# Performance work log

Hardware: AMD Instinct MI355X
Metric: run time of the kernel (lower is better)

## Reference

```python
import math
import jax, jax.numpy as jnp
import numpy as np

NTYPE, C, H, E = 3, 256, 8, 32  # n_embd=256, n_head=8, edge_dim=32
A1 = 16  # aux_x1 feature dim (aux_x2 dim = E - A1)


def setup_inputs() -> dict:
    key = jax.random.key(0)
    ks = jax.random.split(key, 16)
    B, T1, T2 = 8, 128, 256
    s = 0.02
    return {
        "x1": jax.random.normal(ks[0], (B, T1, C), jnp.float32),
        "x2": jax.random.normal(ks[1], (B, T2, C), jnp.float32),
        "aux_x1": jax.random.normal(ks[2], (B, T1, A1), jnp.float32),
        "aux_x2": jax.random.normal(ks[3], (B, T2, E - A1), jnp.float32),
        "masks": jax.random.randint(ks[4], (NTYPE, B, T1, T2), 0, 2, jnp.int32),
        # per-type linear params, stored (in, out) so y = x @ W + b
        "Wq": jax.random.normal(ks[5], (NTYPE, C, C), jnp.float32) * s,
        "bq": jnp.zeros((NTYPE, C), jnp.float32),
        "Wk": jax.random.normal(ks[6], (NTYPE, C + E, C), jnp.float32) * s,
        "bk": jnp.zeros((NTYPE, C), jnp.float32),
        "Wv": jax.random.normal(ks[7], (NTYPE, C + E, C), jnp.float32) * s,
        "bv": jnp.zeros((NTYPE, C), jnp.float32),
        "Wp": jax.random.normal(ks[8], (NTYPE, C, C), jnp.float32) * s,
        "bp": jnp.zeros((NTYPE, C), jnp.float32),
    }


def _aux_attn(x1, x2, aux_x1, aux_x2, mask, Wq, bq, Wk, bk, Wv, bv, Wp, bp):
    """One AuxCrossAttention type. mask: (B,T1,T2) int."""
    B, T1, _ = x1.shape
    T2 = x2.shape[1]
    hd = C // H
    scale = 1.0 / math.sqrt(hd)

    q = x1 @ Wq + bq  # (B,T1,C)
    # k/v over aug_x2 = [x2 | aux_x1 | aux_x2]; split the linear instead of
    # materializing the (B,T1,T2,C+E) concat (same math by linearity).
    Wk_x, Wk_a1, Wk_a2 = Wk[:C], Wk[C:C + A1], Wk[C + A1:]
    Wv_x, Wv_a1, Wv_a2 = Wv[:C], Wv[C:C + A1], Wv[C + A1:]
    k = (x2 @ Wk_x + aux_x2 @ Wk_a2 + bk)[:, None] + (aux_x1 @ Wk_a1)[:, :, None]  # (B,T1,T2,C)
    v = (x2 @ Wv_x + aux_x2 @ Wv_a2 + bv)[:, None] + (aux_x1 @ Wv_a1)[:, :, None]  # (B,T1,T2,C)

    qh = q.reshape(B, T1, H, hd)
    kh = k.reshape(B, T1, T2, H, hd)
    vh = v.reshape(B, T1, T2, H, hd)

    att = jnp.einsum("bthd,btshd->bhts", qh, kh) * scale  # (B,H,T1,T2)
    valid = (mask != 0)[:, None]  # (B,1,T1,T2)
    att = jnp.where(valid, att, -jnp.inf)
    all_masked = (mask == 0).all(-1)  # (B,T1)
    att = jnp.where(all_masked[:, None, :, None], 0.0, att)
    f = jnp.finfo(att.dtype)
    att = jnp.nan_to_num(att, nan=0.0, posinf=f.max, neginf=f.min)
    att = jax.nn.softmax(att, axis=-1)

    y = jnp.einsum("bhts,btshd->bthd", att, vh).reshape(B, T1, C)
    return y @ Wp + bp


def reference(x1, x2, aux_x1, aux_x2, masks, Wq, bq, Wk, bk, Wv, bv, Wp, bp):
    resid = jnp.zeros_like(x1)
    for i in range(NTYPE):
        resid = resid + _aux_attn(x1, x2, aux_x1, aux_x2, masks[i],
                                  Wq[i], bq[i], Wk[i], bk[i], Wv[i], bv[i], Wp[i], bp[i])
    return resid
```

## Files before the change

### kernel.cpp

```cpp
#include <hip/hip_runtime.h>
#include <hip/hip_bf16.h>

#define NC 256
#define HD 32

typedef __attribute__((ext_vector_type(8))) short short8;
typedef __attribute__((ext_vector_type(4))) short short4v;
typedef __attribute__((ext_vector_type(4))) float f32x4;

#define QSC (0.17677669529663687f * 1.4426950408889634f)

__device__ __forceinline__ unsigned short f2bf(float f) {
    union { float f; unsigned u; } v; v.f = f;
    unsigned r = v.u + 0x7fffu + ((v.u >> 16) & 1u);
    return (unsigned short)(r >> 16);
}
__device__ __forceinline__ short8 cvt8(float4 a, float4 b) {
    short8 s;
    s[0] = (short)f2bf(a.x); s[1] = (short)f2bf(a.y);
    s[2] = (short)f2bf(a.z); s[3] = (short)f2bf(a.w);
    s[4] = (short)f2bf(b.x); s[5] = (short)f2bf(b.y);
    s[6] = (short)f2bf(b.z); s[7] = (short)f2bf(b.w);
    return s;
}

__global__ __launch_bounds__(256) void prep(
    const float* __restrict__ x1, const float* __restrict__ x2,
    const float* __restrict__ ax1, const float* __restrict__ ax2,
    const int* __restrict__ masks,
    const float* __restrict__ Wq, const float* __restrict__ Wk,
    const float* __restrict__ Wv, const float* __restrict__ Wp,
    short* __restrict__ x1b, short* __restrict__ A2, short* __restrict__ ax1p,
    unsigned int* __restrict__ mb,
    short* __restrict__ WqT, short* __restrict__ WkT, short* __restrict__ WvT,
    short* __restrict__ WpT)
{
    const int bx = blockIdx.x, tid = threadIdx.x;
    const short8 zero8 = {0, 0, 0, 0, 0, 0, 0, 0};

    if (bx < 64) {
        const size_t base = ((size_t)bx * 256 + tid) * 16;
        const float* p = x1 + base;
        float4 a = *(const float4*)p,       b = *(const float4*)(p + 4);
        float4 c = *(const float4*)(p + 8), d = *(const float4*)(p + 12);
        *(short8*)&x1b[base]     = cvt8(a, b);
        *(short8*)&x1b[base + 8] = cvt8(c, d);
    } else if (bx < 352) {
        const int g = (bx - 64) * 256 + tid;
        const int row = g / 36, c8 = g - row * 36;
        short8 s;
        if (c8 < 32) {
            const float* p = x2 + (size_t)row * 256 + c8 * 8;
            s = cvt8(*(const float4*)p, *(const float4*)(p + 4));
        } else if (c8 < 34) {
            const float* p = ax2 + (size_t)row * 16 + (c8 - 32) * 8;
            s = cvt8(*(const float4*)p, *(const float4*)(p + 4));
        } else {
            s = zero8;
        }
        *(short8*)&A2[(size_t)row * 288 + c8 * 8] = s;
    } else if (bx < 356) {
        const int row = (bx - 352) * 256 + tid;
        const float* p = ax1 + (size_t)row * 16;
        float4 a = *(const float4*)p,       b = *(const float4*)(p + 4);
        float4 c = *(const float4*)(p + 8), d = *(const float4*)(p + 12);
        short* o = ax1p + (size_t)row * 32;
        *(short8*)o        = cvt8(a, b);
        *(short8*)(o + 8)  = cvt8(c, d);
        *(short8*)(o + 16) = zero8;
        *(short8*)(o + 24) = zero8;
    } else if (bx < 548) {
        const int r0 = (bx - 356) * 16;
        const int wave = tid >> 6, lane = tid & 63;
        for (int rr = 0; rr < 16; ++rr) {
            const int row = r0 + rr;
            const int mk = masks[(size_t)row * 256 + tid];
            unsigned long long bal = __ballot(mk != 0);
            if (lane == 0) {
                mb[row * 8 + wave * 2 + 0] = (unsigned int)bal;
                mb[row * 8 + wave * 2 + 1] = (unsigned int)(bal >> 32);
            }
        }
    } else if (bx < 644) {
        const int idx = bx - 548, i = idx >> 5, k8 = idx & 31;
        const int n = tid;
        const float* W = Wq + (size_t)i * 256 * 256;
        short8 s;
#pragma unroll
        for (int j = 0; j < 8; ++j) s[j] = (short)f2bf(W[(size_t)(k8 * 8 + j) * 256 + n]);
        *(short8*)&WqT[(size_t)i * 256 * 256 + (size_t)n * 256 + k8 * 8] = s;
    } else if (bx < 860) {
        const int idx0 = bx - 644;
        const int kv = idx0 / 108, idx = idx0 % 108;
        const int i = idx / 36, k8 = idx % 36;
        const int n = tid;
        const float* W = (kv ? Wv : Wk) + (size_t)i * 288 * 256;
        short* O = (kv ? WvT : WkT) + (size_t)i * 256 * 288;
        short8 s;
#pragma unroll
        for (int j = 0; j < 8; ++j) {
            const int kp = k8 * 8 + j;
            const int src = (kp < 256) ? kp : (kp < 272 ? kp + 16 : -1);
            s[j] = (src >= 0) ? (short)f2bf(W[(size_t)src * 256 + n]) : (short)0;
        }
        *(short8*)&O[(size_t)n * 288 + k8 * 8] = s;
    } else {
        const int idx = bx - 860, i = idx >> 5, k8 = idx & 31;
        const int n = tid;
        const float* W = Wp + (size_t)i * 256 * 256;
        short8 s;
#pragma unroll
        for (int j = 0; j < 8; ++j) s[j] = (short)f2bf(W[(size_t)(k8 * 8 + j) * 256 + n]);
        *(short8*)&WpT[(size_t)i * 256 * 256 + (size_t)n * 256 + k8 * 8] = s;
    }
}

__global__ __launch_bounds__(256) void qkv_attn(
    const short* __restrict__ x1b, const short* __restrict__ A2,
    const short* __restrict__ WqT, const short* __restrict__ WkT,
    const short* __restrict__ WvT, const float* __restrict__ Wv,
    const short* __restrict__ WpT,
    const float* __restrict__ bq, const float* __restrict__ bk,
    const float* __restrict__ bv, const unsigned int* __restrict__ mb,
    short* __restrict__ yb, short* __restrict__ WeffT)
{
    const int tid = threadIdx.x;
    const int wave = tid >> 6, lane = tid & 63;
    const int qd = lane >> 4, ml = lane & 15;
    const int bx = blockIdx.x;

    if (bx == 192) {
        f32x4 wacc[4];
#pragma unroll
        for (int nt = 0; nt < 4; ++nt) wacc[nt] = {0.f, 0.f, 0.f, 0.f};
        for (int i = 0; i < 3; ++i) {
            const float* Wvp = Wv + (size_t)i * 288 * 256;
            const short* Wpt = WpT + (size_t)i * 256 * 256;
            for (int step = 0; step < 8; ++step) {
                const float* ap = Wvp + (size_t)(256 + ml) * 256 + step * 32 + qd * 8;
                short8 af = cvt8(*(const float4*)ap, *(const float4*)(ap + 4));
#pragma unroll
                for (int nt = 0; nt < 4; ++nt) {
                    const int n = (wave * 4 + nt) * 16 + ml;
                    short8 bf = *(const short8*)&Wpt[(size_t)n * 256 + step * 32 + qd * 8];
                    wacc[nt] = __builtin_amdgcn_mfma_f32_16x16x32_bf16(af, bf, wacc[nt], 0, 0, 0);
                }
            }
        }
#pragma unroll
        for (int nt = 0; nt < 4; ++nt) {
            const int n = (wave * 4 + nt) * 16 + ml;
#pragma unroll
            for (int r = 0; r < 4; ++r) {
                WeffT[n * 32 + qd * 4 + r] = (short)f2bf(wacc[nt][r]);
                WeffT[n * 32 + 16 + qd * 4 + r] = 0;
            }
        }
        return;
    }

    const int i = bx >> 6, b = (bx >> 3) & 7, h = bx & 7;
    const size_t bb = (size_t)i * 8 + b;
    const int hc = h * 32;

    __shared__ short q_s[128][40];
    __shared__ short k_s[256][40];
    __shared__ short vT_s[32][264];
    __shared__ short P_s[4][4096];

    const short* Wq_i = WqT + (size_t)i * 256 * 256;
    const short* Wk_i = WkT + (size_t)i * 256 * 288;
    const short* Wv_i = WvT + (size_t)i * 256 * 288;

    {
        f32x4 acc[2][2];
#pragma unroll
        for (int mt = 0; mt < 2; ++mt)
#pragma unroll
            for (int nt = 0; nt < 2; ++nt) acc[mt][nt] = {0.f, 0.f, 0.f, 0.f};
        for (int step = 0; step < 8; ++step) {
            short8 af[2], bf[2];
#pragma unroll
            for (int mt = 0; mt < 2; ++mt)
                af[mt] = *(const short8*)&x1b[(size_t)(b * 128 + wave * 32 + mt * 16 + ml) * 256 + step * 32 + qd * 8];
#pragma unroll
            for (int nt = 0; nt < 2; ++nt)
                bf[nt] = *(const short8*)&Wq_i[(size_t)(hc + nt * 16 + ml) * 256 + step * 32 + qd * 8];
#pragma unroll
            for (int mt = 0; mt < 2; ++mt)
#pragma unroll
                for (int nt = 0; nt < 2; ++nt)
                    acc[mt][nt] = __builtin_amdgcn_mfma_f32_16x16x32_bf16(af[mt], bf[nt], acc[mt][nt], 0, 0, 0);
        }
#pragma unroll
        for (int nt = 0; nt < 2; ++nt) {
            const float bsv = bq[i * 256 + hc + nt * 16 + ml];
#pragma unroll
            for (int mt = 0; mt < 2; ++mt) {
                const int r0 = wave * 32 + mt * 16 + qd * 4;
#pragma unroll
                for (int r = 0; r < 4; ++r)
                    q_s[r0 + r][nt * 16 + ml] = (short)f2bf((acc[mt][nt][r] + bsv) * QSC);
            }
        }
    }

    {
        f32x4 acc[4][2];
#pragma unroll
        for (int mt = 0; mt < 4; ++mt)
#pragma unroll
            for (int nt = 0; nt < 2; ++nt) acc[mt][nt] = {0.f, 0.f, 0.f, 0.f};
        for (int step = 0; step < 9; ++step) {
            short8 af[4], bf[2];
#pragma unroll
            for (int mt = 0; mt < 4; ++mt)
                af[mt] = *(const short8*)&A2[(size_t)(b * 256 + wave * 64 + mt * 16 + ml) * 288 + step * 32 + qd * 8];
#pragma unroll
            for (int nt = 0; nt < 2; ++nt)
                bf[nt] = *(const short8*)&Wk_i[(size_t)(hc + nt * 16 + ml) * 288 + step * 32 + qd * 8];
#pragma unroll
            for (int mt = 0; mt < 4; ++mt)
#pragma unroll
                for (int nt = 0; nt < 2; ++nt)
                    acc[mt][nt] = __builtin_amdgcn_mfma_f32_16x16x32_bf16(af[mt], bf[nt], acc[mt][nt], 0, 0, 0);
        }
#pragma unroll
        for (int nt = 0; nt < 2; ++nt) {
            const float bsv = bk[i * 256 + hc + nt * 16 + ml];
#pragma unroll
            for (int mt = 0; mt < 4; ++mt) {
                const int s0 = wave * 64 + mt * 16 + qd * 4;
#pragma unroll
                for (int r = 0; r < 4; ++r)
                    k_s[s0 + r][nt * 16 + ml] = (short)f2bf(acc[mt][nt][r] + bsv);
            }
        }
    }

    {
        f32x4 acc[4][2];
#pragma unroll
        for (int mt = 0; mt < 4; ++mt)
#pragma unroll
            for (int nt = 0; nt < 2; ++nt) acc[mt][nt] = {0.f, 0.f, 0.f, 0.f};
        for (int step = 0; step < 9; ++step) {
            short8 af[4], bf[2];
#pragma unroll
            for (int mt = 0; mt < 4; ++mt)
                af[mt] = *(const short8*)&A2[(size_t)(b * 256 + wave * 64 + mt * 16 + ml) * 288 + step * 32 + qd * 8];
#pragma unroll
            for (int nt = 0; nt < 2; ++nt)
                bf[nt] = *(const short8*)&Wv_i[(size_t)(hc + nt * 16 + ml) * 288 + step * 32 + qd * 8];
#pragma unroll
            for (int mt = 0; mt < 4; ++mt)
#pragma unroll
                for (int nt = 0; nt < 2; ++nt)
                    acc[mt][nt] = __builtin_amdgcn_mfma_f32_16x16x32_bf16(af[mt], bf[nt], acc[mt][nt], 0, 0, 0);
        }
#pragma unroll
        for (int nt = 0; nt < 2; ++nt) {
            const float bsv = bv[i * 256 + hc + nt * 16 + ml];
#pragma unroll
            for (int mt = 0; mt < 4; ++mt) {
                const int s0 = wave * 64 + mt * 16 + qd * 4;
                short4v s;
                s.x = (short)f2bf(acc[mt][nt][0] + bsv);
                s.y = (short)f2bf(acc[mt][nt][1] + bsv);
                s.z = (short)f2bf(acc[mt][nt][2] + bsv);
                s.w = (short)f2bf(acc[mt][nt][3] + bsv);
                *(short4v*)&vT_s[nt * 16 + ml][s0] = s;
            }
        }
    }
    __syncthreads();

    short* Pw = &P_s[wave][0];
    for (int mt = 0; mt < 2; ++mt) {
        const int t0 = wave * 32 + mt * 16;
        short8 af = *(const short8*)&q_s[t0 + ml][qd * 8];

        f32x4 sacc[16];
#pragma unroll
        for (int nt = 0; nt < 16; ++nt) sacc[nt] = {0.f, 0.f, 0.f, 0.f};
#pragma unroll
        for (int nt = 0; nt < 16; ++nt) {
            short8 bf = *(const short8*)&k_s[nt * 16 + ml][qd * 8];
            sacc[nt] = __builtin_amdgcn_mfma_f32_16x16x32_bf16(af, bf, sacc[nt], 0, 0, 0);
        }

        const int tb = t0 + qd * 4;
        uint4 wlo[4], whi[4];
#pragma unroll
        for (int r = 0; r < 4; ++r) {
            const unsigned int* p = mb + (bb * 128 + tb + r) * 8;
            wlo[r] = *(const uint4*)p;
            whi[r] = *(const uint4*)(p + 4);
        }

        f32x4 rs = {0.f, 0.f, 0.f, 0.f};
#pragma unroll
        for (int nt = 0; nt < 16; ++nt) {
#pragma unroll
            for (int r = 0; r < 4; ++r) {
                unsigned int w;
                switch (nt >> 1) {
                    case 0: w = wlo[r].x; break; case 1: w = wlo[r].y; break;
                    case 2: w = wlo[r].z; break; case 3: w = wlo[r].w; break;
                    case 4: w = whi[r].x; break; case 5: w = whi[r].y; break;
                    case 6: w = whi[r].z; break; default: w = whi[r].w; break;
                }
                const bool mk = (w >> ((nt & 1) * 16 + ml)) & 1u;
                float e = mk ? __builtin_amdgcn_exp2f(sacc[nt][r]) : 0.f;
                sacc[nt][r] = e;
                rs[r] += e;
            }
        }
#pragma unroll
        for (int off = 1; off <= 8; off <<= 1) {
#pragma unroll
            for (int r = 0; r < 4; ++r) rs[r] += __shfl_xor(rs[r], off);
        }
        f32x4 pinv, pfill;
#pragma unroll
        for (int r = 0; r < 4; ++r) {
            const bool z = (rs[r] == 0.f);
            pinv[r]  = z ? 0.f : 1.f / rs[r];
            pfill[r] = z ? (1.f / 256.f) : 0.f;
        }

#pragma unroll
        for (int nt = 0; nt < 16; ++nt) {
            const int sgrp = 2 * nt + (ml >> 3);
            const int pos = ml & 7;
#pragma unroll
            for (int r = 0; r < 4; ++r) {
                const float p = sacc[nt][r] * pinv[r] + pfill[r];
                Pw[(sgrp * 16 + qd * 4 + r) * 8 + pos] = (short)f2bf(p);
            }
        }

        f32x4 oacc[2];
        oacc[0] = {0.f, 0.f, 0.f, 0.f};
        oacc[1] = {0.f, 0.f, 0.f, 0.f};
#pragma unroll
        for (int ks = 0; ks < 8; ++ks) {
            short8 pa = *(const short8*)&Pw[((ks * 4 + qd) * 16 + ml) * 8];
#pragma unroll
            for (int n2 = 0; n2 < 2; ++n2) {
                short8 vf = *(const short8*)&vT_s[n2 * 16 + ml][ks * 32 + qd * 8];
                oacc[n2] = __builtin_amdgcn_mfma_f32_16x16x32_bf16(pa, vf, oacc[n2], 0, 0, 0);
            }
        }

#pragma unroll
        for (int n2 = 0; n2 < 2; ++n2) {
            const int d = hc + n2 * 16 + ml;
#pragma unroll
            for (int r = 0; r < 4; ++r)
                yb[(size_t)(bb * 128 + tb + r) * 256 + d] = (short)f2bf(oacc[n2][r]);
        }
    }
}

__global__ __launch_bounds__(256) void proj2(
    const short* __restrict__ yb, const short* __restrict__ WpT,
    const short* __restrict__ ax1p, const short* __restrict__ WeffT,
    const float* __restrict__ bp, float* __restrict__ out)
{
    const int bx = blockIdx.x;
    const int m0 = (bx >> 2) * 16, n0 = (bx & 3) * 64;
    const int tid = threadIdx.x;
    const int wave = tid >> 6, lane = tid & 63;
    const int qd = lane >> 4, ml = lane & 15;
    const int col = n0 + wave * 16 + ml;

    f32x4 acc = {0.f, 0.f, 0.f, 0.f};

    for (int i = 0; i < 3; ++i) {
        const short* A = yb + (size_t)i * 1024 * 256;
        const short* W = WpT + (size_t)i * 256 * 256;
#pragma unroll
        for (int step = 0; step < 8; ++step) {
            short8 af = *(const short8*)&A[(size_t)(m0 + ml) * 256 + step * 32 + qd * 8];
            short8 bf = *(const short8*)&W[(size_t)col * 256 + step * 32 + qd * 8];
            acc = __builtin_amdgcn_mfma_f32_16x16x32_bf16(af, bf, acc, 0, 0, 0);
        }
    }
    {
        short8 af = *(const short8*)&ax1p[(size_t)(m0 + ml) * 32 + qd * 8];
        short8 bf = *(const short8*)&WeffT[(size_t)col * 32 + qd * 8];
        acc = __builtin_amdgcn_mfma_f32_16x16x32_bf16(af, bf, acc, 0, 0, 0);
    }
    const float b3 = bp[col] + bp[256 + col] + bp[512 + col];
    const int row0 = m0 + qd * 4;
#pragma unroll
    for (int r = 0; r < 4; ++r)
        out[(size_t)(row0 + r) * 256 + col] = acc[r] + b3;
}

extern "C" void kernel_launch(void* const* d_in, const int* in_sizes, int n_in,
                              void* d_out, int out_size, void* d_ws, size_t ws_size,
                              hipStream_t stream)
{
    const float* x1  = (const float*)d_in[0];
    const float* x2  = (const float*)d_in[1];
    const float* ax1 = (const float*)d_in[2];
    const float* ax2 = (const float*)d_in[3];
    const int*   mk  = (const int*)d_in[4];
    const float* Wq  = (const float*)d_in[5];
    const float* bq  = (const float*)d_in[6];
    const float* Wk  = (const float*)d_in[7];
    const float* bk  = (const float*)d_in[8];
    const float* Wv  = (const float*)d_in[9];
    const float* bv  = (const float*)d_in[10];
    const float* Wp  = (const float*)d_in[11];
    const float* bp  = (const float*)d_in[12];

    char* w = (char*)d_ws;
    short* x1b   = (short*)(w + 0);
    short* A2    = (short*)(w + 524288);
    short* ax1p  = (short*)(w + 1703936);
    short* WqT   = (short*)(w + 1769472);
    short* WkT   = (short*)(w + 2162688);
    short* WvT   = (short*)(w + 2605056);
    short* WpT   = (short*)(w + 3047424);
    unsigned int* mbits = (unsigned int*)(w + 3440640);
    short* WeffT = (short*)(w + 3538944);
    short* yb    = (short*)(w + 3555328);

    prep<<<dim3(956), 256, 0, stream>>>(x1, x2, ax1, ax2, mk, Wq, Wk, Wv, Wp,
                                        x1b, A2, ax1p, mbits, WqT, WkT, WvT, WpT);
    qkv_attn<<<dim3(193), 256, 0, stream>>>(x1b, A2, WqT, WkT, WvT, Wv, WpT,
                                            bq, bk, bv, mbits, yb, WeffT);
    proj2<<<dim3(256), 256, 0, stream>>>(yb, WpT, ax1p, WeffT, bp, (float*)d_out);
}
```

Baseline: 115.9 us.

## Fuse Q/K/V projection loops and halve per-wave P scratch buffer

Merges the three separate Q, K and V projection GEMM loops into one loop that shares the A2 fragment loads between K and V and interleaves Q's MFMAs. This avoids loading A2 twice and gives more independent MFMA chains per iteration. The mask words are now loaded before the QK^T MFMAs so their latency overlaps compute. P is written and consumed in two halves, which halves the shared P scratch and lowers LDS use. The cost is more live accumulator registers (Q, K and V at once), which could raise VGPR pressure and reduce occupancy.

```diff
diff --git a/kernel.cpp b/kernel.cpp
--- a/kernel.cpp
+++ b/kernel.cpp
@@ -166,111 +166,101 @@
     __shared__ short q_s[128][40];
     __shared__ short k_s[256][40];
     __shared__ short vT_s[32][264];
-    __shared__ short P_s[4][4096];
+    __shared__ short P_s[4][2048];
 
     const short* Wq_i = WqT + (size_t)i * 256 * 256;
     const short* Wk_i = WkT + (size_t)i * 256 * 288;
     const short* Wv_i = WvT + (size_t)i * 256 * 288;
 
+    f32x4 qacc[2][2], kacc[4][2], vacc[4][2];
+#pragma unroll
+    for (int mt = 0; mt < 2; ++mt)
+#pragma unroll
+        for (int nt = 0; nt < 2; ++nt) qacc[mt][nt] = {0.f, 0.f, 0.f, 0.f};
+#pragma unroll
+    for (int mt = 0; mt < 4; ++mt)
+#pragma unroll
+        for (int nt = 0; nt < 2; ++nt) {
+            kacc[mt][nt] = {0.f, 0.f, 0.f, 0.f};
+            vacc[mt][nt] = {0.f, 0.f, 0.f, 0.f};
+        }
+
+    for (int step = 0; step < 8; ++step) {
+        short8 afq[2], bfq[2], af[4], bfk[2], bfv[2];
+#pragma unroll
+        for (int mt = 0; mt < 2; ++mt)
+            afq[mt] = *(const short8*)&x1b[(size_t)(b * 128 + wave * 32 + mt * 16 + ml) * 256 + step * 32 + qd * 8];
+#pragma unroll
+        for (int nt = 0; nt < 2; ++nt)
+            bfq[nt] = *(const short8*)&Wq_i[(size_t)(hc + nt * 16 + ml) * 256 + step * 32 + qd * 8];
+#pragma unroll
+        for (int mt = 0; mt < 4; ++mt)
+            af[mt] = *(const short8*)&A2[(size_t)(b * 256 + wave * 64 + mt * 16 + ml) * 288 + step * 32 + qd * 8];
+#pragma unroll
+        for (int nt = 0; nt < 2; ++nt) {
+            bfk[nt] = *(const short8*)&Wk_i[(size_t)(hc + nt * 16 + ml) * 288 + step * 32 + qd * 8];
+            bfv[nt] = *(const short8*)&Wv_i[(size_t)(hc + nt * 16 + ml) * 288 + step * 32 + qd * 8];
+        }
+#pragma unroll
+        for (int mt = 0; mt < 2; ++mt)
+#pragma unroll
+            for (int nt = 0; nt < 2; ++nt)
+                qacc[mt][nt] = __builtin_amdgcn_mfma_f32_16x16x32_bf16(afq[mt], bfq[nt], qacc[mt][nt], 0, 0, 0);
+#pragma unroll
+        for (int mt = 0; mt < 4; ++mt)
+#pragma unroll
+            for (int nt = 0; nt < 2; ++nt) {
+                kacc[mt][nt] = __builtin_amdgcn_mfma_f32_16x16x32_bf16(af[mt], bfk[nt], kacc[mt][nt], 0, 0, 0);
+                vacc[mt][nt] = __builtin_amdgcn_mfma_f32_16x16x32_bf16(af[mt], bfv[nt], vacc[mt][nt], 0, 0, 0);
+            }
+    }
     {
-        f32x4 acc[2][2];
-#pragma unroll
-        for (int mt = 0; mt < 2; ++mt)
-#pragma unroll
-            for (int nt = 0; nt < 2; ++nt) acc[mt][nt] = {0.f, 0.f, 0.f, 0.f};
-        for (int step = 0; step < 8; ++step) {
-            short8 af[2], bf[2];
-#pragma unroll
-            for (int mt = 0; mt < 2; ++mt)
-                af[mt] = *(const short8*)&x1b[(size_t)(b * 128 + wave * 32 + mt * 16 + ml) * 256 + step * 32 + qd * 8];
-#pragma unroll
-            for (int nt = 0; nt < 2; ++nt)
-                bf[nt] = *(const short8*)&Wq_i[(size_t)(hc + nt * 16 + ml) * 256 + step * 32 + qd * 8];
-#pragma unroll
-            for (int mt = 0; mt < 2; ++mt)
-#pragma unroll
-                for (int nt = 0; nt < 2; ++nt)
-                    acc[mt][nt] = __builtin_amdgcn_mfma_f32_16x16x32_bf16(af[mt], bf[nt], acc[mt][nt], 0, 0, 0);
-        }
+        const int step = 8;
+        short8 af[4], bfk[2], bfv[2];
+#pragma unroll
+        for (int mt = 0; mt < 4; ++mt)
+            af[mt] = *(const short8*)&A2[(size_t)(b * 256 + wave * 64 + mt * 16 + ml) * 288 + step * 32 + qd * 8];
 #pragma unroll
         for (int nt = 0; nt < 2; ++nt) {
-            const float bsv = bq[i * 256 + hc + nt * 16 + ml];
-#pragma unroll
-            for (int mt = 0; mt < 2; ++mt) {
-                const int r0 = wave * 32 + mt * 16 + qd * 4;
-#pragma unroll
-                for (int r = 0; r < 4; ++r)
-                    q_s[r0 + r][nt * 16 + ml] = (short)f2bf((acc[mt][nt][r] + bsv) * QSC);
-            }
-        }
-    }
-
-    {
-        f32x4 acc[4][2];
+            bfk[nt] = *(const short8*)&Wk_i[(size_t)(hc + nt * 16 + ml) * 288 + step * 32 + qd * 8];
+            bfv[nt] = *(const short8*)&Wv_i[(size_t)(hc + nt * 16 + ml) * 288 + step * 32 + qd * 8];
+        }
 #pragma unroll
         for (int mt = 0; mt < 4; ++mt)
 #pragma unroll
-            for (int nt = 0; nt < 2; ++nt) acc[mt][nt] = {0.f, 0.f, 0.f, 0.f};
-        for (int step = 0; step < 9; ++step) {
-            short8 af[4], bf[2];
-#pragma unroll
-            for (int mt = 0; mt < 4; ++mt)
-                af[mt] = *(const short8*)&A2[(size_t)(b * 256 + wave * 64 + mt * 16 + ml) * 288 + step * 32 + qd * 8];
-#pragma unroll
-            for (int nt = 0; nt < 2; ++nt)
-                bf[nt] = *(const short8*)&Wk_i[(size_t)(hc + nt * 16 + ml) * 288 + step * 32 + qd * 8];
-#pragma unroll
-            for (int mt = 0; mt < 4; ++mt)
-#pragma unroll
-                for (int nt = 0; nt < 2; ++nt)
-                    acc[mt][nt] = __builtin_amdgcn_mfma_f32_16x16x32_bf16(af[mt], bf[nt], acc[mt][nt], 0, 0, 0);
-        }
-#pragma unroll
-        for (int nt = 0; nt < 2; ++nt) {
-            const float bsv = bk[i * 256 + hc + nt * 16 + ml];
-#pragma unroll
-            for (int mt = 0; mt < 4; ++mt) {
-                const int s0 = wave * 64 + mt * 16 + qd * 4;
-#pragma unroll
-                for (int r = 0; r < 4; ++r)
-                    k_s[s0 + r][nt * 16 + ml] = (short)f2bf(acc[mt][nt][r] + bsv);
-            }
-        }
-    }
-
-    {
-        f32x4 acc[4][2];
-#pragma unroll
-        for (int mt = 0; mt < 4; ++mt)
-#pragma unroll
-            for (int nt = 0; nt < 2; ++nt) acc[mt][nt] = {0.f, 0.f, 0.f, 0.f};
-        for (int step = 0; step < 9; ++step) {
-            short8 af[4], bf[2];
-#pragma unroll
-            for (int mt = 0; mt < 4; ++mt)
-                af[mt] = *(const short8*)&A2[(size_t)(b * 256 + wave * 64 + mt * 16 + ml) * 288 + step * 32 + qd * 8];
-#pragma unroll
-            for (int nt = 0; nt < 2; ++nt)
-                bf[nt] = *(const short8*)&Wv_i[(size_t)(hc + nt * 16 + ml) * 288 + step * 32 + qd * 8];
-#pragma unroll
-            for (int mt = 0; mt < 4; ++mt)
-#pragma unroll
-                for (int nt = 0; nt < 2; ++nt)
-                    acc[mt][nt] = __builtin_amdgcn_mfma_f32_16x16x32_bf16(af[mt], bf[nt], acc[mt][nt], 0, 0, 0);
-        }
-#pragma unroll
-        for (int nt = 0; nt < 2; ++nt) {
-            const float bsv = bv[i * 256 + hc + nt * 16 + ml];
-#pragma unroll
-            for (int mt = 0; mt < 4; ++mt) {
-                const int s0 = wave * 64 + mt * 16 + qd * 4;
-                short4v s;
-                s.x = (short)f2bf(acc[mt][nt][0] + bsv);
-                s.y = (short)f2bf(acc[mt][nt][1] + bsv);
-                s.z = (short)f2bf(acc[mt][nt][2] + bsv);
-                s.w = (short)f2bf(acc[mt][nt][3] + bsv);
-                *(short4v*)&vT_s[nt * 16 + ml][s0] = s;
-            }
+            for (int nt = 0; nt < 2; ++nt) {
+                kacc[mt][nt] = __builtin_amdgcn_mfma_f32_16x16x32_bf16(af[mt], bfk[nt], kacc[mt][nt], 0, 0, 0);
+                vacc[mt][nt] = __builtin_amdgcn_mfma_f32_16x16x32_bf16(af[mt], bfv[nt], vacc[mt][nt], 0, 0, 0);
+            }
+    }
+
+#pragma unroll
+    for (int nt = 0; nt < 2; ++nt) {
+        const float bsq = bq[i * 256 + hc + nt * 16 + ml];
+#pragma unroll
+        for (int mt = 0; mt < 2; ++mt) {
+            const int r0 = wave * 32 + mt * 16 + qd * 4;
+#pragma unroll
+            for (int r = 0; r < 4; ++r)
+                q_s[r0 + r][nt * 16 + ml] = (short)f2bf((qacc[mt][nt][r] + bsq) * QSC);
+        }
+    }
+#pragma unroll
+    for (int nt = 0; nt < 2; ++nt) {
+        const float bsk = bk[i * 256 + hc + nt * 16 + ml];
+        const float bsvv = bv[i * 256 + hc + nt * 16 + ml];
+#pragma unroll
+        for (int mt = 0; mt < 4; ++mt) {
+            const int s0 = wave * 64 + mt * 16 + qd * 4;
+#pragma unroll
+            for (int r = 0; r < 4; ++r)
+                k_s[s0 + r][nt * 16 + ml] = (short)f2bf(kacc[mt][nt][r] + bsk);
+            short4v s;
+            s.x = (short)f2bf(vacc[mt][nt][0] + bsvv);
+            s.y = (short)f2bf(vacc[mt][nt][1] + bsvv);
+            s.z = (short)f2bf(vacc[mt][nt][2] + bsvv);
+            s.w = (short)f2bf(vacc[mt][nt][3] + bsvv);
+            *(short4v*)&vT_s[nt * 16 + ml][s0] = s;
         }
     }
     __syncthreads();
@@ -278,24 +268,25 @@
     short* Pw = &P_s[wave][0];
     for (int mt = 0; mt < 2; ++mt) {
         const int t0 = wave * 32 + mt * 16;
-        short8 af = *(const short8*)&q_s[t0 + ml][qd * 8];
-
-        f32x4 sacc[16];
-#pragma unroll
-        for (int nt = 0; nt < 16; ++nt) sacc[nt] = {0.f, 0.f, 0.f, 0.f};
-#pragma unroll
-        for (int nt = 0; nt < 16; ++nt) {
-            short8 bf = *(const short8*)&k_s[nt * 16 + ml][qd * 8];
-            sacc[nt] = __builtin_amdgcn_mfma_f32_16x16x32_bf16(af, bf, sacc[nt], 0, 0, 0);
-        }
-
         const int tb = t0 + qd * 4;
+
         uint4 wlo[4], whi[4];
 #pragma unroll
         for (int r = 0; r < 4; ++r) {
             const unsigned int* p = mb + (bb * 128 + tb + r) * 8;
             wlo[r] = *(const uint4*)p;
             whi[r] = *(const uint4*)(p + 4);
+        }
+
+        short8 af = *(const short8*)&q_s[t0 + ml][qd * 8];
+
+        f32x4 sacc[16];
+#pragma unroll
+        for (int nt = 0; nt < 16; ++nt) sacc[nt] = {0.f, 0.f, 0.f, 0.f};
+#pragma unroll
+        for (int nt = 0; nt < 16; ++nt) {
+            short8 bf = *(const short8*)&k_s[nt * 16 + ml][qd * 8];
+            sacc[nt] = __builtin_amdgcn_mfma_f32_16x16x32_bf16(af, bf, sacc[nt], 0, 0, 0);
         }
 
         f32x4 rs = {0.f, 0.f, 0.f, 0.f};
@@ -329,27 +320,31 @@
             pfill[r] = z ? (1.f / 256.f) : 0.f;
         }
 
-#pragma unroll
-        for (int nt = 0; nt < 16; ++nt) {
-            const int sgrp = 2 * nt + (ml >> 3);
-            const int pos = ml & 7;
-#pragma unroll
-            for (int r = 0; r < 4; ++r) {
-                const float p = sacc[nt][r] * pinv[r] + pfill[r];
-                Pw[(sgrp * 16 + qd * 4 + r) * 8 + pos] = (short)f2bf(p);
-            }
-        }
-
         f32x4 oacc[2];
         oacc[0] = {0.f, 0.f, 0.f, 0.f};
         oacc[1] = {0.f, 0.f, 0.f, 0.f};
 #pragma unroll
-        for (int ks = 0; ks < 8; ++ks) {
-            short8 pa = *(const short8*)&Pw[((ks * 4 + qd) * 16 + ml) * 8];
-#pragma unroll
-            for (int n2 = 0; n2 < 2; ++n2) {
-                short8 vf = *(const short8*)&vT_s[n2 * 16 + ml][ks * 32 + qd * 8];
-                oacc[n2] = __builtin_amdgcn_mfma_f32_16x16x32_bf16(pa, vf, oacc[n2], 0, 0, 0);
+        for (int half = 0; half < 2; ++half) {
+#pragma unroll
+            for (int nt8 = 0; nt8 < 8; ++nt8) {
+                const int nt = half * 8 + nt8;
+                const int sgrp = 2 * nt8 + (ml >> 3);
+                const int pos = ml & 7;
+#pragma unroll
+                for (int r = 0; r < 4; ++r) {
+                    const float p = sacc[nt][r] * pinv[r] + pfill[r];
+                    Pw[(sgrp * 16 + qd * 4 + r) * 8 + pos] = (short)f2bf(p);
+                }
+            }
+#pragma unroll
+            for (int ksl = 0; ksl < 4; ++ksl) {
+                const int ks = half * 4 + ksl;
+                short8 pa = *(const short8*)&Pw[((ksl * 4 + qd) * 16 + ml) * 8];
+#pragma unroll
+                for (int n2 = 0; n2 < 2; ++n2) {
+                    short8 vf = *(const short8*)&vT_s[n2 * 16 + ml][ks * 32 + qd * 8];
+                    oacc[n2] = __builtin_amdgcn_mfma_f32_16x16x32_bf16(pa, vf, oacc[n2], 0, 0, 0);
+                }
             }
         }
 
```

New measurement: 116.0 us. Within noise of the previous version (+0.1%).
